# Kernel optimization log

Measured on AMD Instinct MI355X. Metric: run time of the kernel, lower is better.

## Reference

```python
import jax, jax.numpy as jnp
import numpy as np


def _smooth_l1(x, y):
    # PyTorch F.smooth_l1_loss elementwise with beta=1.0
    d = jnp.abs(x - y)
    return jnp.where(d < 1.0, 0.5 * d * d, d - 0.5)


def setup_inputs() -> dict:
    key = jax.random.key(0)
    k1, k2, k3 = jax.random.split(key, 3)
    B, S, N, D = 2, 8, 2048, 3
    X_v = jax.random.normal(k1, (B, S, N, D), dtype=jnp.float32)
    target_X_v = jax.random.normal(k2, (B, S, N, D), dtype=jnp.float32)
    weights = jax.random.uniform(k3, (B, S), dtype=jnp.float32)
    return {"X_v": X_v, "target_X_v": target_X_v, "weights": weights}


def reference(X_v, target_X_v, weights):
    B, S, N, D = X_v.shape
    # Pairwise squared distances via ||p||^2 + ||t||^2 - 2 p.t  -> [B,S,N,N]
    p2 = jnp.sum(X_v * X_v, axis=-1)            # [B,S,N]
    t2 = jnp.sum(target_X_v * target_X_v, axis=-1)
    cross = jnp.einsum('bsnd,bsmd->bsnm', X_v, target_X_v)
    dist = p2[..., :, None] + t2[..., None, :] - 2.0 * cross
    # Chamfer nearest-neighbor indices (argmin is non-differentiable, as in torch)
    minv = jnp.argmin(dist, axis=-1)   # for each pred point: nearest target [B,S,N]
    minvy = jnp.argmin(dist, axis=-2)  # for each target point: nearest pred
    tagp = jnp.take_along_axis(target_X_v, minv[..., None], axis=2)   # [B,S,N,3]
    predd = jnp.take_along_axis(X_v, minvy[..., None], axis=2)
    tmp1 = jnp.mean(_smooth_l1(X_v, tagp), axis=(-1, -2))       # [B,S]
    tmp2 = jnp.mean(_smooth_l1(target_X_v, predd), axis=(-1, -2))
    per_set = tmp1 + tmp2
    loss = jnp.sum(per_set * weights) / B
    # Centroid loss
    prec = jnp.mean(X_v, axis=2)        # [B,S,3]
    tarc = jnp.mean(target_X_v, axis=2)
    lossc = jnp.sum(_smooth_l1(prec, tarc)) / (B * 3)
    return (loss, lossc)
```

## Files before the change

### kernel.cpp

```cpp
#include <hip/hip_runtime.h>
#include <math.h>

#define N_PTS 2048
#define N_SETS 16
#define B_VAL 2.0f
#define BLOCK 256
#define SEGS 16
#define CPS (N_PTS / SEGS)
#define QPT 8

__device__ __forceinline__ float sl1(float d) {
    d = fabsf(d);
    return d < 1.0f ? 0.5f * d * d : d - 0.5f;
}

__global__ __launch_bounds__(BLOCK) void chamfer_partial(
    const float* __restrict__ X, const float* __restrict__ T,
    float2* __restrict__ ws, float* __restrict__ out)
{
    const int seg = blockIdx.x;
    const int set = blockIdx.y;
    const int dir = blockIdx.z;
    const int tid = threadIdx.x;

    if (seg == 0 && set == 0 && dir == 0 && tid == 0) {
        out[0] = 0.0f;
        out[1] = 0.0f;
    }

    const float* psrc = (dir == 0) ? (X + (size_t)set * N_PTS * 3)
                                   : (T + (size_t)set * N_PTS * 3);
    const float* csrc = (dir == 0) ? (T + (size_t)set * N_PTS * 3)
                                   : (X + (size_t)set * N_PTS * 3);

    __shared__ float4 cand[CPS];
    if (tid < CPS) {
        const int g = seg * CPS + tid;
        float cx = csrc[g * 3 + 0];
        float cy = csrc[g * 3 + 1];
        float cz = csrc[g * 3 + 2];
        cand[tid] = make_float4(cx, cy, cz, cx * cx + cy * cy + cz * cz);
    }
    __syncthreads();

    float ax[QPT], ay[QPT], az[QPT];
    float best[QPT];
    int   bidx[QPT];
#pragma unroll
    for (int j = 0; j < QPT; ++j) {
        const int q = tid + BLOCK * j;
        ax[j] = -2.0f * psrc[q * 3 + 0];
        ay[j] = -2.0f * psrc[q * 3 + 1];
        az[j] = -2.0f * psrc[q * 3 + 2];
        best[j] = INFINITY;
        bidx[j] = 0;
    }

#pragma unroll 4
    for (int m = 0; m < CPS; ++m) {
        float4 c = cand[m];
#pragma unroll
        for (int j = 0; j < QPT; ++j) {
            float d = fmaf(ax[j], c.x, fmaf(ay[j], c.y, fmaf(az[j], c.z, c.w)));
            if (d < best[j]) { best[j] = d; bidx[j] = m; }
        }
    }

    float2* wq = ws + ((size_t)((set * 2 + dir) * SEGS + seg) << 11);
#pragma unroll
    for (int j = 0; j < QPT; ++j) {
        const int q = tid + BLOCK * j;
        float2 v;
        v.x = best[j];
        v.y = __uint_as_float((unsigned int)(seg * CPS + bidx[j]));
        wq[q] = v;
    }
}

__global__ __launch_bounds__(BLOCK) void finalize_kernel(
    const float* __restrict__ X, const float* __restrict__ T,
    const float* __restrict__ W, const float2* __restrict__ ws,
    float* __restrict__ out)
{
    const int chunk = blockIdx.x;
    const int set   = blockIdx.y;
    const int dir   = blockIdx.z;
    const int tid   = threadIdx.x;

    if (chunk == N_PTS / BLOCK) {
        if (dir != 0) return;
        const float* xb = X + (size_t)set * N_PTS * 3;
        const float* tb = T + (size_t)set * N_PTS * 3;
        float acc[6] = {0, 0, 0, 0, 0, 0};
        for (int i = tid; i < N_PTS; i += BLOCK) {
            acc[0] += xb[i * 3 + 0];
            acc[1] += xb[i * 3 + 1];
            acc[2] += xb[i * 3 + 2];
            acc[3] += tb[i * 3 + 0];
            acc[4] += tb[i * 3 + 1];
            acc[5] += tb[i * 3 + 2];
        }
#pragma unroll
        for (int k = 0; k < 6; ++k)
            for (int off = 32; off > 0; off >>= 1)
                acc[k] += __shfl_down(acc[k], off, 64);
        __shared__ float red[4][6];
        if ((tid & 63) == 0)
#pragma unroll
            for (int k = 0; k < 6; ++k) red[tid >> 6][k] = acc[k];
        __syncthreads();
        if (tid == 0) {
            const float inv = 1.0f / (float)N_PTS;
            float l = 0.0f;
#pragma unroll
            for (int k = 0; k < 3; ++k) {
                float a = (red[0][k] + red[1][k] + red[2][k] + red[3][k]) * inv;
                float b = (red[0][k+3] + red[1][k+3] + red[2][k+3] + red[3][k+3]) * inv;
                l += sl1(a - b);
            }
            atomicAdd(&out[1], l * (1.0f / (B_VAL * 3.0f)));
        }
        return;
    }

    const int n = chunk * BLOCK + tid;
    const float* psrc = (dir == 0) ? (X + (size_t)set * N_PTS * 3)
                                   : (T + (size_t)set * N_PTS * 3);
    const float* csrc = (dir == 0) ? (T + (size_t)set * N_PTS * 3)
                                   : (X + (size_t)set * N_PTS * 3);

    const float2* wq = ws + ((size_t)((set * 2 + dir) * SEGS) << 11);
    float bestd = INFINITY;
    unsigned int idx = 0;
#pragma unroll
    for (int s = 0; s < SEGS; ++s) {
        float2 v = wq[((size_t)s << 11) + n];
        if (v.x < bestd) { bestd = v.x; idx = __float_as_uint(v.y); }
    }

    float s = sl1(psrc[n * 3 + 0] - csrc[idx * 3 + 0])
            + sl1(psrc[n * 3 + 1] - csrc[idx * 3 + 1])
            + sl1(psrc[n * 3 + 2] - csrc[idx * 3 + 2]);

    __shared__ float wpart[4];
    for (int off = 32; off > 0; off >>= 1)
        s += __shfl_down(s, off, 64);
    if ((tid & 63) == 0) wpart[tid >> 6] = s;
    __syncthreads();
    if (tid == 0) {
        float tot = wpart[0] + wpart[1] + wpart[2] + wpart[3];
        atomicAdd(&out[0], W[set] * tot * (1.0f / (N_PTS * 3.0f * B_VAL)));
    }
}

extern "C" void kernel_launch(void* const* d_in, const int* in_sizes, int n_in,
                              void* d_out, int out_size, void* d_ws, size_t ws_size,
                              hipStream_t stream) {
    const float* X = (const float*)d_in[0];
    const float* T = (const float*)d_in[1];
    const float* W = (const float*)d_in[2];
    float* out = (float*)d_out;
    float2* ws = (float2*)d_ws;

    chamfer_partial<<<dim3(SEGS, N_SETS, 2), BLOCK, 0, stream>>>(X, T, ws, out);
    finalize_kernel<<<dim3(N_PTS / BLOCK + 1, N_SETS, 2), BLOCK, 0, stream>>>(X, T, W, ws, out);
}
```

Baseline: 84.96 us.

## Fuse chamfer partial and finalize into one kernel via last-block atomic counters

Merges the two-kernel pipeline into one kernel. The last segment block of each group, found through an atomic counter in the workspace, reduces the per-segment minima and computes the smooth-L1 term. A second counter picks the final block, which writes both outputs directly. Centroids are computed from the query registers already loaded by the seg-0 blocks. This removes a kernel launch and the separate centroid pass, but adds a memset launch plus threadfences and serialized tail work in the last blocks.

```diff
diff --git a/kernel.cpp b/kernel.cpp
--- a/kernel.cpp
+++ b/kernel.cpp
@@ -8,25 +8,28 @@
 #define SEGS 16
 #define CPS (N_PTS / SEGS)
 #define QPT 8
+#define NGRP (N_SETS * 2)
+
+#define CTRL_OFF ((size_t)NGRP * SEGS * N_PTS * sizeof(float2))
 
 __device__ __forceinline__ float sl1(float d) {
     d = fabsf(d);
     return d < 1.0f ? 0.5f * d * d : d - 0.5f;
 }
 
-__global__ __launch_bounds__(BLOCK) void chamfer_partial(
+__global__ __launch_bounds__(BLOCK) void chamfer_fused(
     const float* __restrict__ X, const float* __restrict__ T,
-    float2* __restrict__ ws, float* __restrict__ out)
+    const float* __restrict__ W, float2* __restrict__ ws,
+    float* __restrict__ out)
 {
     const int seg = blockIdx.x;
     const int set = blockIdx.y;
     const int dir = blockIdx.z;
     const int tid = threadIdx.x;
+    const int g   = set * 2 + dir;
 
-    if (seg == 0 && set == 0 && dir == 0 && tid == 0) {
-        out[0] = 0.0f;
-        out[1] = 0.0f;
-    }
+    unsigned int* ctrl = (unsigned int*)((char*)ws + CTRL_OFF);
+    float* ctrlf = (float*)ctrl;
 
     const float* psrc = (dir == 0) ? (X + (size_t)set * N_PTS * 3)
                                    : (T + (size_t)set * N_PTS * 3);
@@ -35,10 +38,10 @@
 
     __shared__ float4 cand[CPS];
     if (tid < CPS) {
-        const int g = seg * CPS + tid;
-        float cx = csrc[g * 3 + 0];
-        float cy = csrc[g * 3 + 1];
-        float cz = csrc[g * 3 + 2];
+        const int gidx = seg * CPS + tid;
+        float cx = csrc[gidx * 3 + 0];
+        float cy = csrc[gidx * 3 + 1];
+        float cz = csrc[gidx * 3 + 2];
         cand[tid] = make_float4(cx, cy, cz, cx * cx + cy * cy + cz * cz);
     }
     __syncthreads();
@@ -66,7 +69,7 @@
         }
     }
 
-    float2* wq = ws + ((size_t)((set * 2 + dir) * SEGS + seg) << 11);
+    float2* wq = ws + ((size_t)(g * SEGS + seg) << 11);
 #pragma unroll
     for (int j = 0; j < QPT; ++j) {
         const int q = tid + BLOCK * j;
@@ -75,81 +78,93 @@
         v.y = __uint_as_float((unsigned int)(seg * CPS + bidx[j]));
         wq[q] = v;
     }
-}
 
-__global__ __launch_bounds__(BLOCK) void finalize_kernel(
-    const float* __restrict__ X, const float* __restrict__ T,
-    const float* __restrict__ W, const float2* __restrict__ ws,
-    float* __restrict__ out)
-{
-    const int chunk = blockIdx.x;
-    const int set   = blockIdx.y;
-    const int dir   = blockIdx.z;
-    const int tid   = threadIdx.x;
-
-    if (chunk == N_PTS / BLOCK) {
-        if (dir != 0) return;
-        const float* xb = X + (size_t)set * N_PTS * 3;
-        const float* tb = T + (size_t)set * N_PTS * 3;
-        float acc[6] = {0, 0, 0, 0, 0, 0};
-        for (int i = tid; i < N_PTS; i += BLOCK) {
-            acc[0] += xb[i * 3 + 0];
-            acc[1] += xb[i * 3 + 1];
-            acc[2] += xb[i * 3 + 2];
-            acc[3] += tb[i * 3 + 0];
-            acc[4] += tb[i * 3 + 1];
-            acc[5] += tb[i * 3 + 2];
+    __shared__ float red[4][3];
+    if (seg == 0) {
+        float s0 = 0.f, s1 = 0.f, s2 = 0.f;
+#pragma unroll
+        for (int j = 0; j < QPT; ++j) { s0 += ax[j]; s1 += ay[j]; s2 += az[j]; }
+        for (int off = 32; off > 0; off >>= 1) {
+            s0 += __shfl_down(s0, off, 64);
+            s1 += __shfl_down(s1, off, 64);
+            s2 += __shfl_down(s2, off, 64);
         }
-#pragma unroll
-        for (int k = 0; k < 6; ++k)
-            for (int off = 32; off > 0; off >>= 1)
-                acc[k] += __shfl_down(acc[k], off, 64);
-        __shared__ float red[4][6];
-        if ((tid & 63) == 0)
-#pragma unroll
-            for (int k = 0; k < 6; ++k) red[tid >> 6][k] = acc[k];
+        if ((tid & 63) == 0) {
+            red[tid >> 6][0] = s0; red[tid >> 6][1] = s1; red[tid >> 6][2] = s2;
+        }
         __syncthreads();
         if (tid == 0) {
-            const float inv = 1.0f / (float)N_PTS;
-            float l = 0.0f;
 #pragma unroll
-            for (int k = 0; k < 3; ++k) {
-                float a = (red[0][k] + red[1][k] + red[2][k] + red[3][k]) * inv;
-                float b = (red[0][k+3] + red[1][k+3] + red[2][k+3] + red[3][k+3]) * inv;
-                l += sl1(a - b);
-            }
-            atomicAdd(&out[1], l * (1.0f / (B_VAL * 3.0f)));
+            for (int k = 0; k < 3; ++k)
+                ctrlf[65 + g * 3 + k] =
+                    -0.5f * (red[0][k] + red[1][k] + red[2][k] + red[3][k]);
         }
-        return;
     }
 
-    const int n = chunk * BLOCK + tid;
-    const float* psrc = (dir == 0) ? (X + (size_t)set * N_PTS * 3)
-                                   : (T + (size_t)set * N_PTS * 3);
-    const float* csrc = (dir == 0) ? (T + (size_t)set * N_PTS * 3)
-                                   : (X + (size_t)set * N_PTS * 3);
+    __threadfence();
+    __syncthreads();
+    __shared__ int slast;
+    if (tid == 0) {
+        unsigned int t = atomicAdd(&ctrl[g], 1u);
+        slast = (t == SEGS - 1);
+    }
+    __syncthreads();
+    if (!slast) return;
 
-    const float2* wq = ws + ((size_t)((set * 2 + dir) * SEGS) << 11);
-    float bestd = INFINITY;
-    unsigned int idx = 0;
+    __threadfence();
+    const float2* wp = ws + ((size_t)(g * SEGS) << 11);
+    float lsum = 0.0f;
 #pragma unroll
-    for (int s = 0; s < SEGS; ++s) {
-        float2 v = wq[((size_t)s << 11) + n];
-        if (v.x < bestd) { bestd = v.x; idx = __float_as_uint(v.y); }
+    for (int j = 0; j < QPT; ++j) {
+        const int q = tid + BLOCK * j;
+        float bd = INFINITY;
+        unsigned int idx = 0;
+#pragma unroll
+        for (int s = 0; s < SEGS; ++s) {
+            float2 v = wp[((size_t)s << 11) + q];
+            if (v.x < bd) { bd = v.x; idx = __float_as_uint(v.y); }
+        }
+        const float px = -0.5f * ax[j], py = -0.5f * ay[j], pz = -0.5f * az[j];
+        lsum += sl1(px - csrc[idx * 3 + 0])
+              + sl1(py - csrc[idx * 3 + 1])
+              + sl1(pz - csrc[idx * 3 + 2]);
+    }
+    __shared__ float red2[4];
+    for (int off = 32; off > 0; off >>= 1)
+        lsum += __shfl_down(lsum, off, 64);
+    if ((tid & 63) == 0) red2[tid >> 6] = lsum;
+    __syncthreads();
+    if (tid == 0) {
+        float tot = red2[0] + red2[1] + red2[2] + red2[3];
+        ctrlf[33 + g] = W[set] * tot * (1.0f / (N_PTS * 3.0f * B_VAL));
     }
 
-    float s = sl1(psrc[n * 3 + 0] - csrc[idx * 3 + 0])
-            + sl1(psrc[n * 3 + 1] - csrc[idx * 3 + 1])
-            + sl1(psrc[n * 3 + 2] - csrc[idx * 3 + 2]);
+    __threadfence();
+    __shared__ int slast2;
+    if (tid == 0) {
+        unsigned int t2 = atomicAdd(&ctrl[32], 1u);
+        slast2 = (t2 == NGRP - 1);
+    }
+    __syncthreads();
+    if (!slast2) return;
 
-    __shared__ float wpart[4];
-    for (int off = 32; off > 0; off >>= 1)
-        s += __shfl_down(s, off, 64);
-    if ((tid & 63) == 0) wpart[tid >> 6] = s;
-    __syncthreads();
+    __threadfence();
+    if (tid >= 64) return;
+    float L = (tid < NGRP) ? ctrlf[33 + tid] : 0.0f;
+    float C = 0.0f;
+    if (tid < 48) {
+        const int s = tid / 3, k = tid - s * 3;
+        const float a = ctrlf[65 + (s * 2 + 0) * 3 + k] * (1.0f / N_PTS);
+        const float b = ctrlf[65 + (s * 2 + 1) * 3 + k] * (1.0f / N_PTS);
+        C = sl1(a - b);
+    }
+    for (int off = 32; off > 0; off >>= 1) {
+        L += __shfl_down(L, off, 64);
+        C += __shfl_down(C, off, 64);
+    }
     if (tid == 0) {
-        float tot = wpart[0] + wpart[1] + wpart[2] + wpart[3];
-        atomicAdd(&out[0], W[set] * tot * (1.0f / (N_PTS * 3.0f * B_VAL)));
+        out[0] = L;
+        out[1] = C * (1.0f / (B_VAL * 3.0f));
     }
 }
 
@@ -162,6 +177,6 @@
     float* out = (float*)d_out;
     float2* ws = (float2*)d_ws;
 
-    chamfer_partial<<<dim3(SEGS, N_SETS, 2), BLOCK, 0, stream>>>(X, T, ws, out);
-    finalize_kernel<<<dim3(N_PTS / BLOCK + 1, N_SETS, 2), BLOCK, 0, stream>>>(X, T, W, ws, out);
+    hipMemsetAsync((char*)d_ws + CTRL_OFF, 0, 256, stream);
+    chamfer_fused<<<dim3(SEGS, N_SETS, 2), BLOCK, 0, stream>>>(X, T, W, ws, out);
 }
```

Result: slower. 185.3 us (+118.2%).
